# Kernel tuning notes

Measured on AMD Instinct MI355X. Metric: run time of the kernel, lower is better.

Reference implementation:

```python
import jax, jax.numpy as jnp
import numpy as np

N_NODES = 50000
N_EDGES = 800000
IN_CH = 1024
OUT_CH = 256


def setup_inputs() -> dict:
    key = jax.random.key(0)
    ks = jax.random.split(key, 7)
    x = jax.random.normal(ks[0], (N_NODES, IN_CH), dtype=jnp.float32)
    src_index = jax.random.randint(ks[1], (N_EDGES,), 0, N_NODES, dtype=jnp.int32)
    tar_index = jax.random.randint(ks[2], (N_EDGES,), 0, N_NODES, dtype=jnp.int32)
    edge_weight = jax.random.uniform(ks[3], (N_EDGES,), dtype=jnp.float32)
    self_edge_weight = jax.random.uniform(ks[4], (N_NODES,), dtype=jnp.float32)
    # Linear layer params (torch.nn.Linear: y = x @ W.T + b)
    bound = 1.0 / np.sqrt(IN_CH)
    W = jax.random.uniform(ks[5], (OUT_CH, IN_CH), dtype=jnp.float32, minval=-bound, maxval=bound)
    b = jax.random.uniform(ks[6], (OUT_CH,), dtype=jnp.float32, minval=-bound, maxval=bound)
    return {"x": x, "W": W, "b": b, "src_index": src_index, "tar_index": tar_index,
            "edge_weight": edge_weight, "self_edge_weight": self_edge_weight}


def reference(x, W, b, src_index, tar_index, edge_weight, self_edge_weight):
    # dense linear projection: [N, in] -> [N, out]
    h = jnp.einsum('ni,oi->no', x, W) + b
    # edge aggregation: out[t] += w_e * h[src_e]  (SpMM-like gather/scatter)
    msgs = h[src_index] * edge_weight[:, None]          # [E, out]
    agg = jax.ops.segment_sum(msgs, tar_index, num_segments=h.shape[0])
    # self-loop term
    return agg + self_edge_weight[:, None] * h
```

## Files before the change

### kernel.cpp

```cpp
#include <hip/hip_runtime.h>
#include <hip/hip_bf16.h>

#define N_NODES 50000
#define N_EDGES 800000
#define IN_CH 1024
#define OUT_CH 256
#define NBLK 196

typedef __attribute__((ext_vector_type(8))) short bf16x8;
typedef __attribute__((ext_vector_type(4))) float f32x4;

__device__ inline unsigned short f2bf(float f) {
  union { float f; unsigned int u; } v; v.f = f;
  unsigned int r = v.u + 0x7fffu + ((v.u >> 16) & 1u);
  return (unsigned short)(r >> 16);
}
__device__ inline float bf2f(unsigned short u) {
  union { unsigned int u; float f; } v; v.u = ((unsigned int)u) << 16;
  return v.f;
}

__global__ __launch_bounds__(256) void prep(const float* __restrict__ W,
                                            unsigned short* __restrict__ Wb,
                                            int* __restrict__ counts) {
  const int b = blockIdx.x, t = threadIdx.x;
  if (b < 256) {
    const int i4 = (b * 256 + t) * 4;
    float4 f = *(const float4*)(W + i4);
    *(ushort4*)(Wb + i4) = make_ushort4(f2bf(f.x), f2bf(f.y), f2bf(f.z), f2bf(f.w));
  } else {
    const int i = (b - 256) * 256 + t;
    if (i < N_NODES) counts[i] = 0;
  }
}

__global__ __launch_bounds__(256) void gemm_proj(
    const float* __restrict__ X, const unsigned short* __restrict__ Wb,
    const float* __restrict__ bias, unsigned short* __restrict__ Hb)
{
  __shared__ unsigned short lds_a[2][128][32];
  __shared__ unsigned short lds_b[2][128][32];

  const int tid  = threadIdx.x;
  const int lane = tid & 63;
  const int w    = tid >> 6;
  const int wr   = w >> 1, wc = w & 1;
  const int gm0  = blockIdx.x * 128;
  const int gn0  = blockIdx.y * 128;

  const int arow0 = tid >> 3;
  const int acol  = (tid & 7) * 4;
  const int brow0 = tid >> 2;
  const int bq8   = (tid & 3) * 8;

  f32x4 acc[4][4];
  #pragma unroll
  for (int i = 0; i < 4; i++)
    #pragma unroll
    for (int j = 0; j < 4; j++) acc[i][j] = (f32x4)0.0f;

  float4 av[4];
  bf16x8 bv[2];

#define LOAD_STEP(K0)                                                          \
  {                                                                            \
    _Pragma("unroll")                                                          \
    for (int r = 0; r < 4; r++) {                                              \
      const int grow = gm0 + arow0 + r * 32;                                   \
      av[r] = (grow < N_NODES)                                                 \
                  ? *(const float4*)(X + (size_t)grow * IN_CH + (K0) + acol)   \
                  : make_float4(0.f, 0.f, 0.f, 0.f);                           \
    }                                                                          \
    _Pragma("unroll")                                                          \
    for (int r = 0; r < 2; r++) {                                              \
      const int wrow = gn0 + brow0 + r * 64;                                   \
      bv[r] = *(const bf16x8*)(Wb + (size_t)wrow * IN_CH + (K0) + bq8);        \
    }                                                                          \
  }

#define WRITE_STEP(BUF)                                                        \
  {                                                                            \
    _Pragma("unroll")                                                          \
    for (int r = 0; r < 4; r++)                                                \
      *(ushort4*)&lds_a[BUF][arow0 + r * 32][acol] =                           \
          make_ushort4(f2bf(av[r].x), f2bf(av[r].y), f2bf(av[r].z),            \
                       f2bf(av[r].w));                                         \
    _Pragma("unroll")                                                          \
    for (int r = 0; r < 2; r++)                                                \
      *(bf16x8*)&lds_b[BUF][brow0 + r * 64][bq8] = bv[r];                      \
  }

  LOAD_STEP(0);
  WRITE_STEP(0);
  __syncthreads();

  int buf = 0;
  for (int ks = 0; ks < IN_CH / 32; ks++) {
    if (ks + 1 < IN_CH / 32) LOAD_STEP((ks + 1) * 32);

    bf16x8 af[4], bfr[4];
    const int kq8 = (lane >> 4) * 8;
    #pragma unroll
    for (int i = 0; i < 4; i++)
      af[i] = *(const bf16x8*)&lds_a[buf][wr * 64 + i * 16 + (lane & 15)][kq8];
    #pragma unroll
    for (int j = 0; j < 4; j++)
      bfr[j] = *(const bf16x8*)&lds_b[buf][wc * 64 + j * 16 + (lane & 15)][kq8];

    #pragma unroll
    for (int i = 0; i < 4; i++)
      #pragma unroll
      for (int j = 0; j < 4; j++)
        acc[i][j] = __builtin_amdgcn_mfma_f32_16x16x32_bf16(af[i], bfr[j], acc[i][j], 0, 0, 0);

    if (ks + 1 < IN_CH / 32) WRITE_STEP(buf ^ 1);
    __syncthreads();
    buf ^= 1;
  }
#undef LOAD_STEP
#undef WRITE_STEP

  #pragma unroll
  for (int i = 0; i < 4; i++) {
    const int grow_base = gm0 + wr * 64 + i * 16 + ((lane >> 4) << 2);
    #pragma unroll
    for (int r = 0; r < 4; r++) {
      const int grow = grow_base + r;
      if (grow < N_NODES) {
        #pragma unroll
        for (int j = 0; j < 4; j++) {
          const int gcol = gn0 + wc * 64 + j * 16 + (lane & 15);
          Hb[(size_t)grow * OUT_CH + gcol] = f2bf(acc[i][j][r] + bias[gcol]);
        }
      }
    }
  }
}

__global__ __launch_bounds__(256) void hist_kernel(const int* __restrict__ tar,
                                                   int* __restrict__ counts) {
  int e = blockIdx.x * blockDim.x + threadIdx.x;
  if (e < N_EDGES) atomicAdd(&counts[tar[e]], 1);
}

__global__ __launch_bounds__(256) void scan_block(const int* __restrict__ counts,
                                                  int* __restrict__ offsets,
                                                  int* __restrict__ blocksum) {
  __shared__ int wsum[4];
  const int tid = threadIdx.x, lane = tid & 63, wv = tid >> 6;
  const int i = blockIdx.x * 256 + tid;
  const int v = (i < N_NODES) ? counts[i] : 0;
  int s = v;
  #pragma unroll
  for (int off = 1; off < 64; off <<= 1) {
    int t = __shfl_up(s, off, 64);
    if (lane >= off) s += t;
  }
  if (lane == 63) wsum[wv] = s;
  __syncthreads();
  if (tid == 0) {
    int c = 0;
    #pragma unroll
    for (int k = 0; k < 4; k++) { int t = wsum[k]; wsum[k] = c; c += t; }
  }
  __syncthreads();
  const int excl = wsum[wv] + s - v;
  if (i < N_NODES) offsets[i] = excl;
  if (tid == 255) blocksum[blockIdx.x] = excl + v;
}

__global__ __launch_bounds__(256) void scan_sums(int* __restrict__ blocksum,
                                                 int* __restrict__ offsets) {
  __shared__ int wsum[4];
  const int tid = threadIdx.x, lane = tid & 63, wv = tid >> 6;
  const int v = (tid < NBLK) ? blocksum[tid] : 0;
  int s = v;
  #pragma unroll
  for (int off = 1; off < 64; off <<= 1) {
    int t = __shfl_up(s, off, 64);
    if (lane >= off) s += t;
  }
  if (lane == 63) wsum[wv] = s;
  __syncthreads();
  if (tid == 0) {
    int c = 0;
    #pragma unroll
    for (int k = 0; k < 4; k++) { int t = wsum[k]; wsum[k] = c; c += t; }
  }
  __syncthreads();
  const int excl = wsum[wv] + s - v;
  if (tid < NBLK) blocksum[tid] = excl;
  if (tid == 255) offsets[N_NODES] = excl;
}

__global__ __launch_bounds__(256) void finalize_offsets(int* __restrict__ offsets,
                                                        const int* __restrict__ blocksum,
                                                        int* __restrict__ cursor) {
  const int i = blockIdx.x * 256 + threadIdx.x;
  if (i < N_NODES) {
    const int off = offsets[i] + blocksum[i >> 8];
    offsets[i] = off;
    cursor[i] = off;
  }
}

__global__ __launch_bounds__(256) void fill_csr(const int* __restrict__ src,
                                                const int* __restrict__ tar,
                                                const float* __restrict__ ew,
                                                int* __restrict__ cursor,
                                                int2* __restrict__ edata) {
  int e = blockIdx.x * blockDim.x + threadIdx.x;
  if (e >= N_EDGES) return;
  const int t = tar[e];
  const int p = atomicAdd(&cursor[t], 1);
  edata[p] = make_int2(src[e], __float_as_int(ew[e]));
}

__global__ __launch_bounds__(256) void node_agg(
    const unsigned short* __restrict__ Hb, const int* __restrict__ offsets,
    const int2* __restrict__ edata, const float* __restrict__ sw,
    float* __restrict__ OUT)
{
  const int wid = (blockIdx.x * blockDim.x + threadIdx.x) >> 6;
  if (wid >= N_NODES) return;
  const int lane = threadIdx.x & 63;
  const int e0 = offsets[wid];
  const int e1 = offsets[wid + 1];

  float a0 = 0.f, a1 = 0.f, a2 = 0.f, a3 = 0.f;

  for (int base = e0; base < e1; base += 64) {
    const int avail = e1 - base;
    int2 d = make_int2(0, 0);
    if (lane < avail) d = edata[base + lane];
    const int n = (avail < 64) ? avail : 64;
    int j = 0;
    for (; j + 4 <= n; j += 4) {
      const int   s0 = __shfl(d.x, j, 64),     s1 = __shfl(d.x, j + 1, 64);
      const int   s2 = __shfl(d.x, j + 2, 64), s3 = __shfl(d.x, j + 3, 64);
      const float w0 = __int_as_float(__shfl(d.y, j, 64));
      const float w1 = __int_as_float(__shfl(d.y, j + 1, 64));
      const float w2 = __int_as_float(__shfl(d.y, j + 2, 64));
      const float w3 = __int_as_float(__shfl(d.y, j + 3, 64));
      const ushort4 h0 = *(const ushort4*)(Hb + (size_t)s0 * OUT_CH + lane * 4);
      const ushort4 h1 = *(const ushort4*)(Hb + (size_t)s1 * OUT_CH + lane * 4);
      const ushort4 h2 = *(const ushort4*)(Hb + (size_t)s2 * OUT_CH + lane * 4);
      const ushort4 h3 = *(const ushort4*)(Hb + (size_t)s3 * OUT_CH + lane * 4);
      a0 += w0 * bf2f(h0.x) + w1 * bf2f(h1.x) + w2 * bf2f(h2.x) + w3 * bf2f(h3.x);
      a1 += w0 * bf2f(h0.y) + w1 * bf2f(h1.y) + w2 * bf2f(h2.y) + w3 * bf2f(h3.y);
      a2 += w0 * bf2f(h0.z) + w1 * bf2f(h1.z) + w2 * bf2f(h2.z) + w3 * bf2f(h3.z);
      a3 += w0 * bf2f(h0.w) + w1 * bf2f(h1.w) + w2 * bf2f(h2.w) + w3 * bf2f(h3.w);
    }
    for (; j < n; j++) {
      const int   s = __shfl(d.x, j, 64);
      const float wgt = __int_as_float(__shfl(d.y, j, 64));
      const ushort4 h = *(const ushort4*)(Hb + (size_t)s * OUT_CH + lane * 4);
      a0 += wgt * bf2f(h.x); a1 += wgt * bf2f(h.y);
      a2 += wgt * bf2f(h.z); a3 += wgt * bf2f(h.w);
    }
  }

  const float swv = sw[wid];
  const ushort4 hs = *(const ushort4*)(Hb + (size_t)wid * OUT_CH + lane * 4);
  float4 o;
  o.x = a0 + swv * bf2f(hs.x);
  o.y = a1 + swv * bf2f(hs.y);
  o.z = a2 + swv * bf2f(hs.z);
  o.w = a3 + swv * bf2f(hs.w);
  *(float4*)(OUT + (size_t)wid * OUT_CH + lane * 4) = o;
}

extern "C" void kernel_launch(void* const* d_in, const int* in_sizes, int n_in,
                              void* d_out, int out_size, void* d_ws, size_t ws_size,
                              hipStream_t stream) {
  const float* x   = (const float*)d_in[0];
  const float* W   = (const float*)d_in[1];
  const float* b   = (const float*)d_in[2];
  const int*   src = (const int*)d_in[3];
  const int*   tar = (const int*)d_in[4];
  const float* ew  = (const float*)d_in[5];
  const float* sw  = (const float*)d_in[6];
  float* out = (float*)d_out;

  char* ws = (char*)d_ws;
  size_t o = 0;
  unsigned short* Wb = (unsigned short*)(ws + o);
  o += (size_t)OUT_CH * IN_CH * 2;          o = (o + 255) & ~(size_t)255;
  unsigned short* Hb = (unsigned short*)(ws + o);
  o += (size_t)N_NODES * OUT_CH * 2;        o = (o + 255) & ~(size_t)255;
  int* counts   = (int*)(ws + o); o += (size_t)N_NODES * 4;       o = (o + 255) & ~(size_t)255;
  int* offsets  = (int*)(ws + o); o += (size_t)(N_NODES + 1) * 4; o = (o + 255) & ~(size_t)255;
  int* cursor   = (int*)(ws + o); o += (size_t)N_NODES * 4;       o = (o + 255) & ~(size_t)255;
  int* blocksum = (int*)(ws + o); o += (size_t)NBLK * 4;          o = (o + 255) & ~(size_t)255;
  int2* edata   = (int2*)(ws + o);

  prep<<<256 + NBLK, 256, 0, stream>>>(W, Wb, counts);

  dim3 g1((N_NODES + 127) / 128, OUT_CH / 128);
  gemm_proj<<<g1, 256, 0, stream>>>(x, Wb, b, Hb);

  hist_kernel<<<(N_EDGES + 255) / 256, 256, 0, stream>>>(tar, counts);
  scan_block<<<NBLK, 256, 0, stream>>>(counts, offsets, blocksum);
  scan_sums<<<1, 256, 0, stream>>>(blocksum, offsets);
  finalize_offsets<<<NBLK, 256, 0, stream>>>(offsets, blocksum, cursor);
  fill_csr<<<(N_EDGES + 255) / 256, 256, 0, stream>>>(src, tar, ew, cursor, edata);

  const long long nthreads = (long long)N_NODES * 64;
  node_agg<<<(int)((nthreads + 255) / 256), 256, 0, stream>>>(Hb, offsets, edata, sw, out);
}
```

Baseline: 245.3 us.

## Stage GEMM tiles via direct global-to-LDS loads with swizzle, fuse prep with histogram

```diff
diff --git a/kernel.cpp b/kernel.cpp
--- a/kernel.cpp
+++ b/kernel.cpp
@@ -19,26 +19,37 @@
   union { unsigned int u; float f; } v; v.u = ((unsigned int)u) << 16;
   return v.f;
 }
-
-__global__ __launch_bounds__(256) void prep(const float* __restrict__ W,
-                                            unsigned short* __restrict__ Wb,
-                                            int* __restrict__ counts) {
+__device__ inline unsigned int cvtpk_bf16(float a, float b) {
+  unsigned int r;
+  asm("v_cvt_pk_bf16_f32 %0, %1, %2" : "=v"(r) : "v"(a), "v"(b));
+  return r;
+}
+
+#define GLOAD16(SRC, DST)                                                      \
+  __builtin_amdgcn_global_load_lds(                                            \
+      (const __attribute__((address_space(1))) void*)(SRC),                    \
+      (__attribute__((address_space(3))) void*)(DST), 16, 0, 0)
+
+__global__ __launch_bounds__(256) void prep_hist(const float* __restrict__ W,
+                                                 unsigned short* __restrict__ Wb,
+                                                 const int* __restrict__ tar,
+                                                 int* __restrict__ counts) {
   const int b = blockIdx.x, t = threadIdx.x;
   if (b < 256) {
     const int i4 = (b * 256 + t) * 4;
     float4 f = *(const float4*)(W + i4);
     *(ushort4*)(Wb + i4) = make_ushort4(f2bf(f.x), f2bf(f.y), f2bf(f.z), f2bf(f.w));
   } else {
-    const int i = (b - 256) * 256 + t;
-    if (i < N_NODES) counts[i] = 0;
-  }
-}
-
-__global__ __launch_bounds__(256) void gemm_proj(
+    const int e = (b - 256) * 256 + t;
+    if (e < N_EDGES) atomicAdd(&counts[tar[e]], 1);
+  }
+}
+
+__global__ __launch_bounds__(256, 3) void gemm_proj(
     const float* __restrict__ X, const unsigned short* __restrict__ Wb,
     const float* __restrict__ bias, unsigned short* __restrict__ Hb)
 {
-  __shared__ unsigned short lds_a[2][128][32];
+  __shared__ float lds_a[2][128][32];
   __shared__ unsigned short lds_b[2][128][32];
 
   const int tid  = threadIdx.x;
@@ -48,77 +59,85 @@
   const int gm0  = blockIdx.x * 128;
   const int gn0  = blockIdx.y * 128;
 
-  const int arow0 = tid >> 3;
-  const int acol  = (tid & 7) * 4;
-  const int brow0 = tid >> 2;
-  const int bq8   = (tid & 3) * 8;
-
   f32x4 acc[4][4];
   #pragma unroll
   for (int i = 0; i < 4; i++)
     #pragma unroll
     for (int j = 0; j < 4; j++) acc[i][j] = (f32x4)0.0f;
 
-  float4 av[4];
-  bf16x8 bv[2];
-
-#define LOAD_STEP(K0)                                                          \
+#define STAGE(BUF, K0)                                                         \
   {                                                                            \
     _Pragma("unroll")                                                          \
-    for (int r = 0; r < 4; r++) {                                              \
-      const int grow = gm0 + arow0 + r * 32;                                   \
-      av[r] = (grow < N_NODES)                                                 \
-                  ? *(const float4*)(X + (size_t)grow * IN_CH + (K0) + acol)   \
-                  : make_float4(0.f, 0.f, 0.f, 0.f);                           \
+    for (int q = 0; q < 4; q++) {                                              \
+      const int wl   = w * 4 + q;                                              \
+      const int row  = 8 * wl + (lane >> 3);                                   \
+      const int grow = gm0 + row;                                              \
+      const int sc   = (lane & 7) ^ (row & 7);                                 \
+      if (grow < N_NODES)                                                      \
+        GLOAD16(X + (size_t)grow * IN_CH + (K0) + sc * 4,                      \
+                &lds_a[BUF][8 * wl][0]);                                       \
     }                                                                          \
     _Pragma("unroll")                                                          \
-    for (int r = 0; r < 2; r++) {                                              \
-      const int wrow = gn0 + brow0 + r * 64;                                   \
-      bv[r] = *(const bf16x8*)(Wb + (size_t)wrow * IN_CH + (K0) + bq8);        \
+    for (int q = 0; q < 2; q++) {                                              \
+      const int wl  = w * 2 + q;                                               \
+      const int row = 16 * wl + (lane >> 2);                                   \
+      const int sc  = (lane & 3) ^ (row & 3);                                  \
+      GLOAD16(Wb + (size_t)(gn0 + row) * IN_CH + (K0) + sc * 8,                \
+              &lds_b[BUF][16 * wl][0]);                                        \
     }                                                                          \
   }
 
-#define WRITE_STEP(BUF)                                                        \
+#define COMPUTE(BUF)                                                           \
   {                                                                            \
-    _Pragma("unroll")                                                          \
-    for (int r = 0; r < 4; r++)                                                \
-      *(ushort4*)&lds_a[BUF][arow0 + r * 32][acol] =                           \
-          make_ushort4(f2bf(av[r].x), f2bf(av[r].y), f2bf(av[r].z),            \
-                       f2bf(av[r].w));                                         \
-    _Pragma("unroll")                                                          \
-    for (int r = 0; r < 2; r++)                                                \
-      *(bf16x8*)&lds_b[BUF][brow0 + r * 64][bq8] = bv[r];                      \
-  }
-
-  LOAD_STEP(0);
-  WRITE_STEP(0);
-  __syncthreads();
-
-  int buf = 0;
-  for (int ks = 0; ks < IN_CH / 32; ks++) {
-    if (ks + 1 < IN_CH / 32) LOAD_STEP((ks + 1) * 32);
-
-    bf16x8 af[4], bfr[4];
-    const int kq8 = (lane >> 4) * 8;
-    #pragma unroll
-    for (int i = 0; i < 4; i++)
-      af[i] = *(const bf16x8*)&lds_a[buf][wr * 64 + i * 16 + (lane & 15)][kq8];
-    #pragma unroll
-    for (int j = 0; j < 4; j++)
-      bfr[j] = *(const bf16x8*)&lds_b[buf][wc * 64 + j * 16 + (lane & 15)][kq8];
-
-    #pragma unroll
-    for (int i = 0; i < 4; i++)
-      #pragma unroll
-      for (int j = 0; j < 4; j++)
-        acc[i][j] = __builtin_amdgcn_mfma_f32_16x16x32_bf16(af[i], bfr[j], acc[i][j], 0, 0, 0);
-
-    if (ks + 1 < IN_CH / 32) WRITE_STEP(buf ^ 1);
+    const int l15 = lane & 15;                                                 \
+    const int kb  = lane >> 4;                                                 \
+    bf16x8 af[4], bfr[4];                                                      \
+    _Pragma("unroll")                                                          \
+    for (int i = 0; i < 4; i++) {                                              \
+      const int row = wr * 64 + i * 16 + l15;                                  \
+      const int c0  = (2 * kb) ^ (row & 7);                                    \
+      const int c1  = (2 * kb + 1) ^ (row & 7);                                \
+      f32x4 lo = *(const f32x4*)&lds_a[BUF][row][c0 * 4];                      \
+      f32x4 hi = *(const f32x4*)&lds_a[BUF][row][c1 * 4];                      \
+      union { unsigned int u[4]; bf16x8 v; } t;                                \
+      t.u[0] = cvtpk_bf16(lo[0], lo[1]);                                       \
+      t.u[1] = cvtpk_bf16(lo[2], lo[3]);                                       \
+      t.u[2] = cvtpk_bf16(hi[0], hi[1]);                                       \
+      t.u[3] = cvtpk_bf16(hi[2], hi[3]);                                       \
+      af[i] = t.v;                                                             \
+    }                                                                          \
+    _Pragma("unroll")                                                          \
+    for (int j = 0; j < 4; j++) {                                              \
+      const int row = wc * 64 + j * 16 + l15;                                  \
+      const int c   = kb ^ (row & 3);                                          \
+      bfr[j] = *(const bf16x8*)&lds_b[BUF][row][c * 8];                        \
+    }                                                                          \
+    _Pragma("unroll")                                                          \
+    for (int i = 0; i < 4; i++)                                                \
+      _Pragma("unroll")                                                        \
+      for (int j = 0; j < 4; j++)                                              \
+        acc[i][j] = __builtin_amdgcn_mfma_f32_16x16x32_bf16(af[i], bfr[j],     \
+                                                            acc[i][j], 0, 0, 0); \
+  }
+
+  STAGE(0, 0);
+  __syncthreads();
+
+  for (int ks = 0; ks < 32; ks += 2) {
+    if (ks + 1 < 32) STAGE(1, (ks + 1) * 32);
+    COMPUTE(0);
     __syncthreads();
-    buf ^= 1;
-  }
-#undef LOAD_STEP
-#undef WRITE_STEP
+    if (ks + 2 < 32) STAGE(0, (ks + 2) * 32);
+    COMPUTE(1);
+    __syncthreads();
+  }
+#undef STAGE
+#undef COMPUTE
+
+  float bj[4];
+  #pragma unroll
+  for (int j = 0; j < 4; j++)
+    bj[j] = bias[gn0 + wc * 64 + j * 16 + (lane & 15)];
 
   #pragma unroll
   for (int i = 0; i < 4; i++) {
@@ -130,17 +149,11 @@
         #pragma unroll
         for (int j = 0; j < 4; j++) {
           const int gcol = gn0 + wc * 64 + j * 16 + (lane & 15);
-          Hb[(size_t)grow * OUT_CH + gcol] = f2bf(acc[i][j][r] + bias[gcol]);
+          Hb[(size_t)grow * OUT_CH + gcol] = f2bf(acc[i][j][r] + bj[j]);
         }
       }
     }
   }
-}
-
-__global__ __launch_bounds__(256) void hist_kernel(const int* __restrict__ tar,
-                                                   int* __restrict__ counts) {
-  int e = blockIdx.x * blockDim.x + threadIdx.x;
-  if (e < N_EDGES) atomicAdd(&counts[tar[e]], 1);
 }
 
 __global__ __launch_bounds__(256) void scan_block(const int* __restrict__ counts,
@@ -294,17 +307,16 @@
   int* blocksum = (int*)(ws + o); o += (size_t)NBLK * 4;          o = (o + 255) & ~(size_t)255;
   int2* edata   = (int2*)(ws + o);
 
-  prep<<<256 + NBLK, 256, 0, stream>>>(W, Wb, counts);
-
-  dim3 g1((N_NODES + 127) / 128, OUT_CH / 128);
-  gemm_proj<<<g1, 256, 0, stream>>>(x, Wb, b, Hb);
-
-  hist_kernel<<<(N_EDGES + 255) / 256, 256, 0, stream>>>(tar, counts);
+  hipMemsetAsync(counts, 0, (size_t)N_NODES * 4, stream);
+  prep_hist<<<256 + (N_EDGES + 255) / 256, 256, 0, stream>>>(W, Wb, tar, counts);
   scan_block<<<NBLK, 256, 0, stream>>>(counts, offsets, blocksum);
   scan_sums<<<1, 256, 0, stream>>>(blocksum, offsets);
   finalize_offsets<<<NBLK, 256, 0, stream>>>(offsets, blocksum, cursor);
   fill_csr<<<(N_EDGES + 255) / 256, 256, 0, stream>>>(src, tar, ew, cursor, edata);
 
+  dim3 g1((N_NODES + 127) / 128, OUT_CH / 128);
+  gemm_proj<<<g1, 256, 0, stream>>>(x, Wb, b, Hb);
+
   const long long nthreads = (long long)N_NODES * 64;
   node_agg<<<(int)((nthreads + 255) / 256), 256, 0, stream>>>(Hb, offsets, edata, sw, out);
 }
```

Measured after the change: 248.4 us. No clear change (+1.3%).
